# Performance work log

Measured on AMD Instinct MI355X. Metric: run time of the kernel, lower is better.

## Reference

```python
import jax, jax.numpy as jnp
import numpy as np

B, S, T = 64, 128, 64
HD, VS, VT = 1024, 32000, 32000


def setup_inputs() -> dict:
    key = jax.random.key(0)
    ks = jax.random.split(key, 20)
    p = lambda k, shape: (jax.random.normal(k, shape, jnp.float32) * 0.02)
    return {
        "src_nums": jax.random.randint(ks[0], (B, S), 0, VS, dtype=jnp.int32),
        "tgt_nums": jax.random.randint(ks[1], (B, T), 0, VT, dtype=jnp.int32),
        "src_emb": p(ks[2], (VS, HD)),
        "tgt_emb": p(ks[3], (VT, HD)),
        "enc_Wx1": p(ks[4], (HD, 4 * HD)),
        "enc_Wh1": p(ks[5], (HD, 4 * HD)),
        "enc_b1": jnp.zeros((4 * HD,), jnp.float32),
        "enc_Wx2": p(ks[6], (HD, 4 * HD)),
        "enc_Wh2": p(ks[7], (HD, 4 * HD)),
        "enc_b2": jnp.zeros((4 * HD,), jnp.float32),
        "dec_Wx": p(ks[8], (HD, 4 * HD)),
        "dec_Wh": p(ks[9], (HD, 4 * HD)),
        "dec_b": jnp.zeros((4 * HD,), jnp.float32),
        "dec_h0": p(ks[10], (1, HD)),
        "dec_m0": p(ks[11], (1, HD)),
        "Wt": p(ks[12], (2 * HD, HD)),
        "bt": jnp.zeros((HD,), jnp.float32),
        "Wo": p(ks[13], (HD, VT)),
        "bo": jnp.zeros((VT,), jnp.float32),
    }


def _lstm_cell(x, h, c, Wx, Wh, b):
    g = x @ Wx + h @ Wh + b            # [B, 4H], gate order i,f,g,o
    i, f, gg, o = jnp.split(g, 4, axis=-1)
    c = jax.nn.sigmoid(f) * c + jax.nn.sigmoid(i) * jnp.tanh(gg)
    h = jax.nn.sigmoid(o) * jnp.tanh(c)
    return h, c


def reference(src_nums, tgt_nums, src_emb, tgt_emb,
              enc_Wx1, enc_Wh1, enc_b1, enc_Wx2, enc_Wh2, enc_b2,
              dec_Wx, dec_Wh, dec_b, dec_h0, dec_m0, Wt, bt, Wo, bo):
    Bb, Ss = src_nums.shape
    Hd = src_emb.shape[1]
    # ---- Encoder: 2-layer LSTM over source ----
    embs = src_emb[src_nums]                       # [B,S,H]
    z0 = jnp.zeros((Bb, Hd), embs.dtype)

    def enc_step(carry, x):
        h1, c1, h2, c2 = carry
        h1, c1 = _lstm_cell(x, h1, c1, enc_Wx1, enc_Wh1, enc_b1)
        h2, c2 = _lstm_cell(h1, h2, c2, enc_Wx2, enc_Wh2, enc_b2)
        return (h1, c1, h2, c2), h2

    _, Hseq = jax.lax.scan(enc_step, (z0, z0, z0, z0), jnp.swapaxes(embs, 0, 1))
    Henc = jnp.swapaxes(Hseq, 0, 1)                # [B,S,H]
    mask = src_nums == 0                           # pad mask
    scale = 1.0 / jnp.sqrt(jnp.array(Hd, jnp.float32))

    # ---- Decoder: per-step attention + LSTMCell + tanh proj + log-softmax ----
    h = jnp.tile(dec_h0, (Bb, 1))
    m = jnp.tile(dec_m0, (Bb, 1))

    def dec_step(carry, tgt):
        h, m, loss = carry
        scores = jnp.einsum('bd,bsd->bs', h, Henc) * scale
        scores = jnp.where(mask, -jnp.inf, scores)
        a = jax.nn.softmax(scores, axis=-1)
        ctx = jnp.einsum('bs,bsd->bd', a, Henc)
        z = jnp.tanh(jnp.concatenate([ctx, h], axis=-1) @ Wt + bt)
        logp = jax.nn.log_softmax(z @ Wo + bo, axis=-1)    # [B,V]
        tok_lp = jnp.take_along_axis(logp, tgt[:, None], axis=-1)[:, 0]
        loss = loss - jnp.sum(jnp.where(tgt != 0, tok_lp, 0.0))
        x = tgt_emb[tgt]
        h, m = _lstm_cell(x, h, m, dec_Wx, dec_Wh, dec_b)
        return (h, m, loss), None

    (_, _, loss), _ = jax.lax.scan(
        dec_step, (h, m, jnp.float32(0.0)), jnp.swapaxes(tgt_nums, 0, 1))
    return loss
```

## Files before the change

kernel.cpp:

```cpp
#include <hip/hip_runtime.h>


#define Bv 64
#define Sv 128
#define Tv 64
#define Hv 1024
#define H4v 4096
#define Vv 32000
#define NBLK 256

using bf16x8 = __attribute__((ext_vector_type(8))) short;
using f32x4  = __attribute__((ext_vector_type(4))) float;

typedef __attribute__((address_space(1))) const void gvoid_t;
typedef __attribute__((address_space(3))) void lvoid_t;

__device__ __forceinline__ void gload16(const void* g, void* l) {
  __builtin_amdgcn_global_load_lds((gvoid_t*)g, (lvoid_t*)l, 16, 0, 0);
}

__device__ __forceinline__ float bf2f(unsigned short u) {
  unsigned int v = ((unsigned int)u) << 16;
  return __uint_as_float(v);
}
__device__ __forceinline__ unsigned short f2bf(float f) {
  unsigned int u = __float_as_uint(f);
  return (unsigned short)((u + 0x7FFFu + ((u >> 16) & 1u)) >> 16);
}
__device__ __forceinline__ float sigm(float x) { return 1.f / (1.f + __expf(-x)); }
__device__ __forceinline__ float tanh_f(float x) {
  float ax = fabsf(x);
  float e = __expf(-2.f * ax);
  float t = (1.f - e) / (1.f + e);
  return copysignf(t, x);
}

__device__ __forceinline__ int4 ldx4(const unsigned short* p) {
  int4 r;
  asm volatile("global_load_dwordx4 %0, %1, off" : "=v"(r) : "v"(p));
  return r;
}
__device__ __forceinline__ int2 ldx2(const unsigned short* p) {
  int2 r;
  asm volatile("global_load_dwordx2 %0, %1, off" : "=v"(r) : "v"(p));
  return r;
}
__device__ __forceinline__ void st_u16_wt(unsigned short* p, unsigned v) {
  asm volatile("global_store_short %0, %1, off sc0 sc1" :: "v"(p), "v"(v) : "memory");
}
__device__ __forceinline__ void vm_wait(int n) {
  if (n >= 12)     asm volatile("s_waitcnt vmcnt(12)" ::: "memory");
  else if (n >= 8) asm volatile("s_waitcnt vmcnt(8)" ::: "memory");
  else if (n >= 4) asm volatile("s_waitcnt vmcnt(4)" ::: "memory");
  else             asm volatile("s_waitcnt vmcnt(0)" ::: "memory");
}

__device__ __forceinline__ void wait_all64(int* f, int tid) {
  if (tid < 64) {
    int it = 0;
    while (true) {
      int v = __hip_atomic_load(f + tid, __ATOMIC_RELAXED, __HIP_MEMORY_SCOPE_AGENT);
      if (__all(v != 0)) break;
      __builtin_amdgcn_s_sleep(1);
      if (++it > (1 << 17)) break;
    }
  }
  __syncthreads();
}
__device__ __forceinline__ void wait_all128(int* f, int tid) {
  if (tid < 64) {
    int it = 0;
    while (true) {
      int a = __hip_atomic_load(f + tid, __ATOMIC_RELAXED, __HIP_MEMORY_SCOPE_AGENT);
      int b = __hip_atomic_load(f + tid + 64, __ATOMIC_RELAXED, __HIP_MEMORY_SCOPE_AGENT);
      if (__all((a != 0) && (b != 0))) break;
      __builtin_amdgcn_s_sleep(1);
      if (++it > (1 << 17)) break;
    }
  }
  __syncthreads();
}
__device__ __forceinline__ void post_flag(int* f, int tid) {
  __syncthreads();
  if (tid == 0) __hip_atomic_store(f, 1, __ATOMIC_RELAXED, __HIP_MEMORY_SCOPE_AGENT);
}

__global__ __launch_bounds__(256) void transpose_bf16(const float* __restrict__ in,
                                                      unsigned short* __restrict__ out,
                                                      int R, int C, int ostride) {
  __shared__ float tile[32][33];
  int tx = threadIdx.x, ty = threadIdx.y;
  int c0 = blockIdx.x * 32, r0 = blockIdx.y * 32;
#pragma unroll
  for (int i = 0; i < 32; i += 8)
    tile[ty + i][tx] = in[(size_t)(r0 + ty + i) * C + c0 + tx];
  __syncthreads();
#pragma unroll
  for (int i = 0; i < 32; i += 8)
    out[(size_t)(c0 + ty + i) * ostride + r0 + tx] = f2bf(tile[tx][ty + i]);
}

__global__ __launch_bounds__(256) void gather_emb(const int* __restrict__ toks,
                                                  const float* __restrict__ emb,
                                                  unsigned short* __restrict__ dst) {
  int r = blockIdx.x, tid = threadIdx.x;
  int tok = toks[r];
  int j = tid * 4;
  float4 v = *(const float4*)&emb[(size_t)tok * Hv + j];
  ushort4 o;
  o.x = f2bf(v.x); o.y = f2bf(v.y); o.z = f2bf(v.z); o.w = f2bf(v.w);
  *(ushort4*)&dst[(size_t)r * Hv + j] = o;
}

__global__ __launch_bounds__(256) void init_k(unsigned short* __restrict__ zhx,
                                              unsigned short* __restrict__ hdx0,
                                              const float* __restrict__ h0,
                                              int* __restrict__ flg) {
  int idx = blockIdx.x * 256 + threadIdx.x;
  int j = idx & (Hv - 1);
  int b = idx >> 10;
  zhx[idx] = 0;
  hdx0[(j >> 4) * 1024 + b * 16 + (j & 15)] = f2bf(h0[j]);
  if (idx < 28672) flg[idx] = 0;
}

template <int EPI>
__global__ __launch_bounds__(256) void gemm128(const unsigned short* __restrict__ A,
                                               const unsigned short* __restrict__ Bt,
                                               const float* __restrict__ bias,
                                               unsigned short* __restrict__ Cbf,
                                               int M, int N, int K,
                                               float* __restrict__ partial,
                                               float* __restrict__ tlog,
                                               const int* __restrict__ tgt) {
  __shared__ unsigned short As[128 * 64];
  __shared__ unsigned short Bs[128 * 64];
  int tid = threadIdx.x, lane = tid & 63, w = tid >> 6;
  int wr = w >> 1, wc = w & 1;
  int m0 = blockIdx.y * 128, n0 = blockIdx.x * 128;
  f32x4 acc[4][4] = {};
  for (int k0 = 0; k0 < K; k0 += 64) {
    __syncthreads();
#pragma unroll
    for (int q = 0; q < 4; ++q) {
      int idx = q * 256 + tid;
      int row = idx >> 3, phys = idx & 7, lg = phys ^ (row & 7);
      gload16(A + (size_t)(m0 + row) * K + k0 + lg * 8, &As[idx * 8]);
    }
#pragma unroll
    for (int q = 0; q < 4; ++q) {
      int idx = q * 256 + tid;
      int row = idx >> 3, phys = idx & 7, lg = phys ^ (row & 7);
      gload16(Bt + (size_t)(n0 + row) * K + k0 + lg * 8, &Bs[idx * 8]);
    }
    __syncthreads();
#pragma unroll
    for (int kk = 0; kk < 64; kk += 32) {
      int lgb = (kk >> 3) + (lane >> 4);
      bf16x8 af[4], bfr[4];
#pragma unroll
      for (int m = 0; m < 4; ++m) {
        int row = wr * 64 + m * 16 + (lane & 15);
        af[m] = *(const bf16x8*)&As[(row * 8 + (lgb ^ (row & 7))) * 8];
      }
#pragma unroll
      for (int n = 0; n < 4; ++n) {
        int row = wc * 64 + n * 16 + (lane & 15);
        bfr[n] = *(const bf16x8*)&Bs[(row * 8 + (lgb ^ (row & 7))) * 8];
      }
#pragma unroll
      for (int m = 0; m < 4; ++m)
#pragma unroll
        for (int n = 0; n < 4; ++n)
          acc[m][n] = __builtin_amdgcn_mfma_f32_16x16x32_bf16(af[m], bfr[n], acc[m][n], 0, 0, 0);
    }
  }
  if (EPI == 2) {
#pragma unroll
    for (int m = 0; m < 4; ++m)
#pragma unroll
      for (int n = 0; n < 4; ++n) {
        int col = n0 + wc * 64 + n * 16 + (lane & 15);
        float bv = bias[col];
#pragma unroll
        for (int j = 0; j < 4; ++j) {
          int row = m0 + wr * 64 + m * 16 + (lane >> 4) * 4 + j;
          float v = acc[m][n][j] + bv;
          Cbf[(size_t)row * N + col] = f2bf(tanhf(v));
        }
      }
  } else if (EPI == 3) {
    int chunk = (n0 + wc * 64) >> 6;
#pragma unroll
    for (int m = 0; m < 4; ++m)
#pragma unroll
      for (int j = 0; j < 4; ++j) {
        int row = m0 + wr * 64 + m * 16 + (lane >> 4) * 4 + j;
        int tv = tgt[row];
        float se = 0.f;
#pragma unroll
        for (int n = 0; n < 4; ++n) {
          int col = n0 + wc * 64 + n * 16 + (lane & 15);
          float v = acc[m][n][j] + bias[col];
          se += __expf(v);
          if (col == tv) tlog[row] = v;
        }
        se += __shfl_xor(se, 1);
        se += __shfl_xor(se, 2);
        se += __shfl_xor(se, 4);
        se += __shfl_xor(se, 8);
        if ((lane & 15) == 0) partial[(size_t)chunk * M + row] = se;
      }
  } else {
    constexpr int TTc = (EPI == 4) ? 128 : 64;
#pragma unroll
    for (int m = 0; m < 4; ++m)
#pragma unroll
      for (int n = 0; n < 4; ++n) {
        int col = n0 + wc * 64 + n * 16 + (lane & 15);
        float bv = bias[col];
        int hcol = col & 1023, g = col >> 10;
#pragma unroll
        for (int j = 0; j < 4; ++j) {
          int row = m0 + wr * 64 + m * 16 + (lane >> 4) * 4 + j;
          int t = row % TTc, b = row / TTc;
          float v = acc[m][n][j] + bv;
          Cbf[((((size_t)t * 64 + (hcol >> 4)) * 64 + b) * 16 + (hcol & 15)) * 4 + g] = f2bf(v);
        }
      }
  }
}

template <int GRP>
__device__ __forceinline__ void run6(
    int gid, int tid, const unsigned short* __restrict__ Wg,
    const unsigned short* __restrict__ XPC, const float* __restrict__ eb2,
    const float* __restrict__ m0, const unsigned short* __restrict__ ZHX,
    unsigned short* __restrict__ H1X, unsigned short* __restrict__ H2X,
    unsigned short* __restrict__ HDX,
    int* __restrict__ C1, int* __restrict__ C2, int* __restrict__ CD,
    unsigned short* Wl, float* gl) {
  constexpr int COLS = (GRP == 1) ? 8 : 16;
  constexpr int KD   = (GRP == 1) ? 2048 : 1024;
  constexpr int NKS  = KD / 128;
  constexpr int NFR  = (GRP == 1) ? 2 : 4;
  constexpr int NT   = (GRP == 2) ? 63 : 128;
  constexpr int GPR  = KD / 8;
  constexpr int WROWS = 4 * COLS;
  const int lane = tid & 63, w = tid >> 6, l4 = lane >> 4, l15 = lane & 15;
  const int j0 = gid * COLS;

#pragma unroll
  for (int it = 0; it < (WROWS * GPR) / 256; ++it) {
    int L = it * 256 + tid;
    int row = L / GPR;
    int g = (L % GPR) ^ (row & 7);
    int gate = row / COLS, cl = row % COLS;
    gload16(Wg + (size_t)(gate * 1024 + j0 + cl) * KD + g * 8, Wl + (size_t)L * 8);
  }
  const int rr0 = (GRP == 1) ? (tid >> 3) : (tid >> 4);
  const int cc  = (GRP == 1) ? (tid & 7) : (tid & 15);
  const bool cellact = (GRP != 1) || (tid < 128);
  float cst[4];
#pragma unroll
  for (int c = 0; c < 4; ++c) cst[c] = (GRP == 2) ? m0[j0 + cc] : 0.f;
  float br_[4];
  if (GRP == 1) {
#pragma unroll
    for (int g = 0; g < 4; ++g) br_[g] = eb2[g * 1024 + j0 + cc];
  }
  const int kq16 = w * (KD / 32);

  asm volatile("s_waitcnt vmcnt(0)" ::: "memory");
  __syncthreads();

  for (int t = 0; t < NT; ++t) {
    if (GRP == 0) {
      if (t > 0) wait_all64(C1 + (t - 1) * 64, tid);
    } else if (GRP == 1) {
      wait_all64(C1 + t * 64, tid);
      if (t > 0) wait_all128(C2 + (t - 1) * 128, tid);
    } else {
      if (t > 0) wait_all64(CD + t * 64, tid);
    }
    const unsigned short* slab;
    int jb;
    if (GRP == 0) {
      slab = (t == 0) ? ZHX : H1X + (size_t)(t - 1) * 65536;
      jb = w * 256;
    } else if (GRP == 2) {
      slab = HDX + (size_t)t * 65536;
      jb = w * 256;
    } else {
      if (w < 2) { slab = H1X + (size_t)t * 65536; jb = w * 512; }
      else {
        slab = (t == 0) ? ZHX : H2X + (size_t)(t - 1) * 65536;
        jb = w * 512 - 1024;
      }
    }
    int2 xq[4];
    if (GRP != 1) {
      const unsigned short* xb = XPC + ((size_t)t * 64 + gid) * 4096;
#pragma unroll
      for (int c = 0; c < 4; ++c) xq[c] = ldx2(xb + ((c * 16 + rr0) * 16 + cc) * 4);
    }
    const unsigned short* rp[4];
#pragma unroll
    for (int m = 0; m < 4; ++m)
      rp[m] = slab + (size_t)((jb >> 4) + (l4 >> 1)) * 1024 + (m * 16 + l15) * 16 + (l4 & 1) * 8;
    int4 afr[3][4];
#pragma unroll
    for (int pk = 0; pk < 3; ++pk)
#pragma unroll
      for (int m = 0; m < 4; ++m) afr[pk][m] = ldx4(rp[m] + pk * 2048);
    if (GRP != 1) vm_wait(12);
    bf16x8 wb[2][NFR];
#pragma unroll
    for (int n = 0; n < NFR; ++n) {
      int row = n * 16 + l15;
      wb[0][n] = *(const bf16x8*)&Wl[(size_t)row * KD + (size_t)((kq16 + l4) ^ (row & 7)) * 8];
    }
    f32x4 acc[4][NFR] = {};
#pragma unroll
    for (int ks = 0; ks < NKS; ++ks) {
      if (ks + 1 < NKS) {
#pragma unroll
        for (int n = 0; n < NFR; ++n) {
          int row = n * 16 + l15;
          wb[(ks + 1) & 1][n] = *(const bf16x8*)&Wl[(size_t)row * KD +
              (size_t)((kq16 + (ks + 1) * 4 + l4) ^ (row & 7)) * 8];
        }
      }
      int nrem = 4 * (NKS - 1 - ks);
      vm_wait(nrem > 8 ? 8 : nrem);
      __builtin_amdgcn_sched_barrier(0);
#pragma unroll
      for (int m = 0; m < 4; ++m)
#pragma unroll
        for (int n = 0; n < NFR; ++n)
          acc[m][n] = __builtin_amdgcn_mfma_f32_16x16x32_bf16(
              *(const bf16x8*)&afr[ks % 3][m], wb[ks & 1][n], acc[m][n], 0, 0, 0);
      if (ks + 3 < NKS) {
#pragma unroll
        for (int m = 0; m < 4; ++m) afr[ks % 3][m] = ldx4(rp[m] + (ks + 3) * 2048);
      }
    }
    unsigned short* outp;
    if (GRP == 0)      outp = H1X + (size_t)t * 65536 + gid * 1024;
    else if (GRP == 2) outp = HDX + (size_t)(t + 1) * 65536 + gid * 1024;
    else               outp = H2X + (size_t)t * 65536 + (size_t)(j0 >> 4) * 1024 + (j0 & 8);
#pragma unroll
    for (int c = 0; c < 4; ++c) {
#pragma unroll
      for (int n = 0; n < NFR; ++n)
#pragma unroll
        for (int j = 0; j < 4; ++j) {
          int ric = l4 * 4 + j;
          int col = n * 16 + l15;
          gl[(w * 16 + ric) * 64 + (col ^ ((ric * 4) & 63))] = acc[c][n][j];
        }
      __syncthreads();
      if (cellact) {
        float G[4];
#pragma unroll
        for (int g = 0; g < 4; ++g) {
          int sw = (g * COLS + cc) ^ ((rr0 * 4) & 63);
          G[g] = gl[(0 * 16 + rr0) * 64 + sw] + gl[(1 * 16 + rr0) * 64 + sw] +
                 gl[(2 * 16 + rr0) * 64 + sw] + gl[(3 * 16 + rr0) * 64 + sw];
        }
        float gi, gf, gg, go;
        if (GRP == 1) {
          gi = G[0] + br_[0]; gf = G[1] + br_[1]; gg = G[2] + br_[2]; go = G[3] + br_[3];
        } else {
          gi = G[0] + bf2f((unsigned short)(xq[c].x & 0xFFFF));
          gf = G[1] + bf2f((unsigned short)((unsigned)xq[c].x >> 16));
          gg = G[2] + bf2f((unsigned short)(xq[c].y & 0xFFFF));
          go = G[3] + bf2f((unsigned short)((unsigned)xq[c].y >> 16));
        }
        float cn = sigm(gf) * cst[c] + sigm(gi) * tanh_f(gg);
        float hn = sigm(go) * tanh_f(cn);
        cst[c] = cn;
        st_u16_wt(outp + (c * 16 + rr0) * 16 + cc, (unsigned)f2bf(hn));
      }
      __syncthreads();
    }
    asm volatile("s_waitcnt vmcnt(0)" ::: "memory");
    if (GRP == 0)      post_flag(C1 + t * 64 + gid, tid);
    else if (GRP == 1) post_flag(C2 + t * 128 + gid, tid);
    else               post_flag(CD + (t + 1) * 64 + gid, tid);
  }
}

__global__ __launch_bounds__(256, 1) void chain_kernel(
    const unsigned short* __restrict__ W1T, const unsigned short* __restrict__ W2S,
    const unsigned short* __restrict__ WDT, const unsigned short* __restrict__ XPC1,
    const unsigned short* __restrict__ XPCD, const float* __restrict__ eb2,
    const float* __restrict__ m0, const unsigned short* __restrict__ ZHX,
    unsigned short* __restrict__ H1X, unsigned short* __restrict__ H2X,
    unsigned short* __restrict__ HDX, int* __restrict__ flg) {
  __shared__ unsigned short Wl[65536];
  __shared__ float gl[4 * 16 * 64];
  int bid = blockIdx.x, tid = threadIdx.x;
  int* C1 = flg;
  int* C2 = flg + 8192;
  int* CD = flg + 24576;
  if (bid < 64)
    run6<0>(bid, tid, W1T, XPC1, eb2, nullptr, ZHX, H1X, H2X, HDX, C1, C2, CD, Wl, gl);
  else if (bid < 192)
    run6<1>(bid - 64, tid, W2S, nullptr, eb2, nullptr, ZHX, H1X, H2X, HDX, C1, C2, CD, Wl, gl);
  else
    run6<2>(bid - 192, tid, WDT, XPCD, eb2, m0, ZHX, H1X, H2X, HDX, C1, C2, CD, Wl, gl);
}

__global__ __launch_bounds__(256) void reshape_h(const unsigned short* __restrict__ H2X,
                                                 const unsigned short* __restrict__ HDX,
                                                 unsigned short* __restrict__ HENC,
                                                 unsigned short* __restrict__ HDEC) {
  int row = blockIdx.x, tid = threadIdx.x;
  int g = tid >> 2, c = (tid & 3) * 4;
  if (row < Bv * Sv) {
    int b = row >> 7, s = row & 127;
    ushort4 v = *(const ushort4*)&H2X[(size_t)s * 65536 + g * 1024 + b * 16 + c];
    *(ushort4*)&HENC[(size_t)row * Hv + tid * 4] = v;
  } else {
    int r2 = row - Bv * Sv;
    int b = r2 >> 6, t = r2 & 63;
    ushort4 v = *(const ushort4*)&HDX[(size_t)t * 65536 + g * 1024 + b * 16 + c];
    *(ushort4*)&HDEC[(size_t)r2 * Hv + tid * 4] = v;
  }
}

__global__ __launch_bounds__(256) void attn_kernel(const unsigned short* __restrict__ Hdec,
                                                   const unsigned short* __restrict__ Henc,
                                                   const int* __restrict__ src_nums,
                                                   unsigned short* __restrict__ cat) {
  __shared__ float hd[Hv];
  __shared__ float sc[Sv];
  __shared__ float al[Sv];
  __shared__ float inv_s;
  int r = blockIdx.x;
  int b = r >> 6;
  int tid = threadIdx.x;
#pragma unroll
  for (int i = 0; i < 4; ++i) {
    int j = i * 256 + tid;
    hd[j] = bf2f(Hdec[(size_t)r * Hv + j]);
  }
  __syncthreads();
  int lane = tid & 63, w = tid >> 6;
  {
    int s = w * 32 + (lane >> 1);
    int half = lane & 1;
    const unsigned short* hrow = Henc + ((size_t)(b * Sv + s)) * Hv + half * 512;
    const float* hdp = hd + half * 512;
    float ps = 0.f;
#pragma unroll 8
    for (int j = 0; j < 512; j += 2) {
      unsigned int u = *(const unsigned int*)&hrow[j];
      ps += hdp[j] * bf2f((unsigned short)(u & 0xFFFFu));
      ps += hdp[j + 1] * bf2f((unsigned short)(u >> 16));
    }
    ps += __shfl_xor(ps, 1);
    if (half == 0) {
      float v = ps * 0.03125f;
      if (src_nums[b * Sv + s] == 0) v = -1e30f;
      sc[s] = v;
    }
  }
  __syncthreads();
  if (w == 0) {
    float v0 = sc[lane], v1 = sc[lane + 64];
    float mx = fmaxf(v0, v1);
#pragma unroll
    for (int o = 1; o < 64; o <<= 1) mx = fmaxf(mx, __shfl_xor(mx, o));
    float e0 = __expf(v0 - mx), e1 = __expf(v1 - mx);
    al[lane] = e0;
    al[lane + 64] = e1;
    float ss = e0 + e1;
#pragma unroll
    for (int o = 1; o < 64; o <<= 1) ss += __shfl_xor(ss, o);
    if (lane == 0) inv_s = 1.f / ss;
  }
  __syncthreads();
  float inv = inv_s;
  int j0 = tid * 4;
  float a0 = 0, a1 = 0, a2 = 0, a3 = 0;
  for (int s2 = 0; s2 < Sv; ++s2) {
    float a = al[s2];
    const unsigned short* hr = Henc + ((size_t)(b * Sv + s2)) * Hv + j0;
    ushort4 u = *(const ushort4*)hr;
    a0 += a * bf2f(u.x);
    a1 += a * bf2f(u.y);
    a2 += a * bf2f(u.z);
    a3 += a * bf2f(u.w);
  }
  ushort4 o4;
  o4.x = f2bf(a0 * inv); o4.y = f2bf(a1 * inv); o4.z = f2bf(a2 * inv); o4.w = f2bf(a3 * inv);
  *(ushort4*)&cat[(size_t)r * 2048 + j0] = o4;
  ushort4 h4;
  h4.x = f2bf(hd[j0]); h4.y = f2bf(hd[j0 + 1]); h4.z = f2bf(hd[j0 + 2]); h4.w = f2bf(hd[j0 + 3]);
  *(ushort4*)&cat[(size_t)r * 2048 + 1024 + j0] = h4;
}

__global__ __launch_bounds__(256) void loss_row(const float* __restrict__ partial,
                                                const float* __restrict__ tlog,
                                                const int* __restrict__ tgt,
                                                float* __restrict__ rowloss) {
  int r = blockIdx.x * 256 + threadIdx.x;
  float ssum = 0.f;
  for (int c = 0; c < Vv / 64; ++c) ssum += partial[(size_t)c * (Bv * Tv) + r];
  float l = logf(ssum) - tlog[r];
  rowloss[r] = (tgt[r] != 0) ? l : 0.f;
}

__global__ __launch_bounds__(256) void loss_final(const float* __restrict__ rowloss,
                                                  float* __restrict__ out) {
  __shared__ float red[256];
  int tid = threadIdx.x;
  float s = 0.f;
  for (int i = tid; i < Bv * Tv; i += 256) s += rowloss[i];
  red[tid] = s;
  __syncthreads();
  for (int o = 128; o > 0; o >>= 1) {
    if (tid < o) red[tid] += red[tid + o];
    __syncthreads();
  }
  if (tid == 0) out[0] = red[0];
}

extern "C" void kernel_launch(void* const* d_in, const int* in_sizes, int n_in,
                              void* d_out, int out_size, void* d_ws, size_t ws_size,
                              hipStream_t stream) {
  (void)in_sizes; (void)n_in; (void)out_size; (void)ws_size;
  const int* src_nums = (const int*)d_in[0];
  const int* tgt_nums = (const int*)d_in[1];
  const float* src_emb = (const float*)d_in[2];
  const float* tgt_emb = (const float*)d_in[3];
  const float* eWx1 = (const float*)d_in[4];
  const float* eWh1 = (const float*)d_in[5];
  const float* eb1  = (const float*)d_in[6];
  const float* eWx2 = (const float*)d_in[7];
  const float* eWh2 = (const float*)d_in[8];
  const float* eb2  = (const float*)d_in[9];
  const float* dWx  = (const float*)d_in[10];
  const float* dWh  = (const float*)d_in[11];
  const float* db   = (const float*)d_in[12];
  const float* h0   = (const float*)d_in[13];
  const float* m0   = (const float*)d_in[14];
  const float* Wt   = (const float*)d_in[15];
  const float* bt   = (const float*)d_in[16];
  const float* Wo   = (const float*)d_in[17];
  const float* bo   = (const float*)d_in[18];

  char* base = (char*)d_ws;
  size_t off = 0;
  auto alloc = [&](size_t bytes) -> void* {
    void* r = base + off;
    off += (bytes + 255) & ~(size_t)255;
    return r;
  };
  unsigned short* WX1T = (unsigned short*)alloc((size_t)H4v * Hv * 2);
  unsigned short* W1T  = (unsigned short*)alloc((size_t)H4v * Hv * 2);
  unsigned short* W2S  = (unsigned short*)alloc((size_t)H4v * 2048 * 2);
  unsigned short* DWXT = (unsigned short*)alloc((size_t)H4v * Hv * 2);
  unsigned short* WDT  = (unsigned short*)alloc((size_t)H4v * Hv * 2);
  unsigned short* WTT  = (unsigned short*)alloc((size_t)Hv * 2048 * 2);
  unsigned short* WOT  = (unsigned short*)alloc((size_t)Vv * Hv * 2);
  unsigned short* SEMB = (unsigned short*)alloc((size_t)Bv * Sv * Hv * 2);
  unsigned short* TEMB = (unsigned short*)alloc((size_t)Bv * Tv * Hv * 2);
  unsigned short* XPC1 = (unsigned short*)alloc((size_t)Bv * Sv * H4v * 2);
  unsigned short* XPCD = (unsigned short*)alloc((size_t)Bv * Tv * H4v * 2);
  unsigned short* HENC = (unsigned short*)alloc((size_t)Bv * Sv * Hv * 2);
  unsigned short* HDEC = (unsigned short*)alloc((size_t)Bv * Tv * Hv * 2);
  unsigned short* H1X  = (unsigned short*)alloc((size_t)Sv * Bv * Hv * 2);
  unsigned short* H2X  = (unsigned short*)alloc((size_t)Sv * Bv * Hv * 2);
  unsigned short* HDX  = (unsigned short*)alloc((size_t)Tv * Bv * Hv * 2);
  unsigned short* ZHX  = (unsigned short*)alloc((size_t)Bv * Hv * 2);
  unsigned short* CAT  = (unsigned short*)alloc((size_t)Bv * Tv * 2048 * 2);
  unsigned short* ZBUF = (unsigned short*)alloc((size_t)Bv * Tv * Hv * 2);
  float* PART  = (float*)alloc((size_t)(Vv / 64) * (Bv * Tv) * 4);
  float* TLOG  = (float*)alloc((size_t)(Bv * Tv) * 4);
  float* RLOSS = (float*)alloc((size_t)(Bv * Tv) * 4);
  int* FLG     = (int*)alloc(28672 * 4);

  dim3 tb(32, 8);
  transpose_bf16<<<dim3(H4v / 32, Hv / 32), tb, 0, stream>>>(eWx1, WX1T, Hv, H4v, Hv);
  transpose_bf16<<<dim3(H4v / 32, Hv / 32), tb, 0, stream>>>(eWh1, W1T, Hv, H4v, Hv);
  transpose_bf16<<<dim3(H4v / 32, Hv / 32), tb, 0, stream>>>(eWx2, W2S, Hv, H4v, 2048);
  transpose_bf16<<<dim3(H4v / 32, Hv / 32), tb, 0, stream>>>(eWh2, W2S + 1024, Hv, H4v, 2048);
  transpose_bf16<<<dim3(H4v / 32, Hv / 32), tb, 0, stream>>>(dWx, DWXT, Hv, H4v, Hv);
  transpose_bf16<<<dim3(H4v / 32, Hv / 32), tb, 0, stream>>>(dWh, WDT, Hv, H4v, Hv);
  transpose_bf16<<<dim3(Hv / 32, 2048 / 32), tb, 0, stream>>>(Wt, WTT, 2048, Hv, 2048);
  transpose_bf16<<<dim3(Vv / 32, Hv / 32), tb, 0, stream>>>(Wo, WOT, Hv, Vv, Hv);

  init_k<<<256, 256, 0, stream>>>(ZHX, HDX, h0, FLG);
  gather_emb<<<Bv * Sv, 256, 0, stream>>>(src_nums, src_emb, SEMB);
  gather_emb<<<Bv * Tv, 256, 0, stream>>>(tgt_nums, tgt_emb, TEMB);

  gemm128<4><<<dim3(H4v / 128, (Bv * Sv) / 128), 256, 0, stream>>>(
      SEMB, WX1T, eb1, XPC1, Bv * Sv, H4v, Hv, nullptr, nullptr, nullptr);
  gemm128<5><<<dim3(H4v / 128, (Bv * Tv) / 128), 256, 0, stream>>>(
      TEMB, DWXT, db, XPCD, Bv * Tv, H4v, Hv, nullptr, nullptr, nullptr);

  chain_kernel<<<NBLK, 256, 0, stream>>>(W1T, W2S, WDT, XPC1, XPCD, eb2, m0, ZHX, H1X, H2X,
                                         HDX, FLG);

  reshape_h<<<Bv * Sv + Bv * Tv, 256, 0, stream>>>(H2X, HDX, HENC, HDEC);

  attn_kernel<<<Bv * Tv, 256, 0, stream>>>(HDEC, HENC, src_nums, CAT);
  gemm128<2><<<dim3(Hv / 128, (Bv * Tv) / 128), 256, 0, stream>>>(
      CAT, WTT, bt, ZBUF, Bv * Tv, Hv, 2048, nullptr, nullptr, nullptr);
  gemm128<3><<<dim3(Vv / 128, (Bv * Tv) / 128), 256, 0, stream>>>(
      ZBUF, WOT, bo, nullptr, Bv * Tv, Vv, Hv, PART, TLOG, tgt_nums);
  loss_row<<<(Bv * Tv) / 256, 256, 0, stream>>>(PART, TLOG, tgt_nums, RLOSS);
  loss_final<<<1, 256, 0, stream>>>(RLOSS, (float*)d_out);
}
```

Before: 1.832 ms.

## Deepen recurrent A-operand prefetch to eight stages and coalesce hidden-state stores

Inside the persistent LSTM chain kernel, the A-fragment prefetch ring for the recurrent matmul grows from three to eight k-slices, and the vmcnt waits are recomputed to match, so more global loads are in flight on the serial per-timestep critical path. The per-thread 16-bit write-through stores of new hidden values are replaced by staging them in LDS and issuing packed 8-byte write-through stores. This costs more registers for the deeper ring and adds an extra LDS round trip and barrier per step.

```diff
diff --git a/kernel.cpp b/kernel.cpp
--- a/kernel.cpp
+++ b/kernel.cpp
@@ -45,14 +45,20 @@
   asm volatile("global_load_dwordx2 %0, %1, off" : "=v"(r) : "v"(p));
   return r;
 }
-__device__ __forceinline__ void st_u16_wt(unsigned short* p, unsigned v) {
-  asm volatile("global_store_short %0, %1, off sc0 sc1" :: "v"(p), "v"(v) : "memory");
-}
-__device__ __forceinline__ void vm_wait(int n) {
-  if (n >= 12)     asm volatile("s_waitcnt vmcnt(12)" ::: "memory");
-  else if (n >= 8) asm volatile("s_waitcnt vmcnt(8)" ::: "memory");
-  else if (n >= 4) asm volatile("s_waitcnt vmcnt(4)" ::: "memory");
-  else             asm volatile("s_waitcnt vmcnt(0)" ::: "memory");
+__device__ __forceinline__ void stx2u_wt(unsigned short* p, int2 v) {
+  asm volatile("global_store_dwordx2 %0, %1, off sc0 sc1" :: "v"(p), "v"(v) : "memory");
+}
+__device__ __forceinline__ void vm_wait_c(int n) {
+  switch (n) {
+    case 28: asm volatile("s_waitcnt vmcnt(28)" ::: "memory"); break;
+    case 24: asm volatile("s_waitcnt vmcnt(24)" ::: "memory"); break;
+    case 20: asm volatile("s_waitcnt vmcnt(20)" ::: "memory"); break;
+    case 16: asm volatile("s_waitcnt vmcnt(16)" ::: "memory"); break;
+    case 12: asm volatile("s_waitcnt vmcnt(12)" ::: "memory"); break;
+    case 8:  asm volatile("s_waitcnt vmcnt(8)"  ::: "memory"); break;
+    case 4:  asm volatile("s_waitcnt vmcnt(4)"  ::: "memory"); break;
+    default: asm volatile("s_waitcnt vmcnt(0)"  ::: "memory"); break;
+  }
 }
 
 __device__ __forceinline__ void wait_all64(int* f, int tid) {
@@ -232,7 +238,7 @@
 }
 
 template <int GRP>
-__device__ __forceinline__ void run6(
+__device__ __forceinline__ void run7(
     int gid, int tid, const unsigned short* __restrict__ Wg,
     const unsigned short* __restrict__ XPC, const float* __restrict__ eb2,
     const float* __restrict__ m0, const unsigned short* __restrict__ ZHX,
@@ -308,12 +314,11 @@
 #pragma unroll
     for (int m = 0; m < 4; ++m)
       rp[m] = slab + (size_t)((jb >> 4) + (l4 >> 1)) * 1024 + (m * 16 + l15) * 16 + (l4 & 1) * 8;
-    int4 afr[3][4];
-#pragma unroll
-    for (int pk = 0; pk < 3; ++pk)
+    int4 afr[8][4];
+#pragma unroll
+    for (int pk = 0; pk < 8; ++pk)
 #pragma unroll
       for (int m = 0; m < 4; ++m) afr[pk][m] = ldx4(rp[m] + pk * 2048);
-    if (GRP != 1) vm_wait(12);
     bf16x8 wb[2][NFR];
 #pragma unroll
     for (int n = 0; n < NFR; ++n) {
@@ -331,24 +336,24 @@
               (size_t)((kq16 + (ks + 1) * 4 + l4) ^ (row & 7)) * 8];
         }
       }
-      int nrem = 4 * (NKS - 1 - ks);
-      vm_wait(nrem > 8 ? 8 : nrem);
+      vm_wait_c((GRP == 1) ? (ks <= 8 ? 28 : 60 - 4 * ks) : (28 - 4 * ks));
       __builtin_amdgcn_sched_barrier(0);
 #pragma unroll
       for (int m = 0; m < 4; ++m)
 #pragma unroll
         for (int n = 0; n < NFR; ++n)
           acc[m][n] = __builtin_amdgcn_mfma_f32_16x16x32_bf16(
-              *(const bf16x8*)&afr[ks % 3][m], wb[ks & 1][n], acc[m][n], 0, 0, 0);
-      if (ks + 3 < NKS) {
-#pragma unroll
-        for (int m = 0; m < 4; ++m) afr[ks % 3][m] = ldx4(rp[m] + (ks + 3) * 2048);
+              *(const bf16x8*)&afr[ks & 7][m], wb[ks & 1][n], acc[m][n], 0, 0, 0);
+      if (GRP == 1 && ks < 8) {
+#pragma unroll
+        for (int m = 0; m < 4; ++m) afr[ks & 7][m] = ldx4(rp[m] + (ks + 8) * 2048);
       }
     }
     unsigned short* outp;
     if (GRP == 0)      outp = H1X + (size_t)t * 65536 + gid * 1024;
     else if (GRP == 2) outp = HDX + (size_t)(t + 1) * 65536 + gid * 1024;
     else               outp = H2X + (size_t)t * 65536 + (size_t)(j0 >> 4) * 1024 + (j0 & 8);
+    unsigned short ho[4];
 #pragma unroll
     for (int c = 0; c < 4; ++c) {
 #pragma unroll
@@ -380,9 +385,30 @@
         float cn = sigm(gf) * cst[c] + sigm(gi) * tanh_f(gg);
         float hn = sigm(go) * tanh_f(cn);
         cst[c] = cn;
-        st_u16_wt(outp + (c * 16 + rr0) * 16 + cc, (unsigned)f2bf(hn));
+        ho[c] = f2bf(hn);
       }
       __syncthreads();
+    }
+    unsigned short* hb = (unsigned short*)gl;
+    if (cellact) {
+#pragma unroll
+      for (int c = 0; c < 4; ++c) hb[(c * 16 + rr0) * COLS + cc] = ho[c];
+    }
+    __syncthreads();
+    if (GRP != 1) {
+      int b2 = tid >> 2, q4 = (tid & 3) * 4;
+      ushort4 hv = *(const ushort4*)&hb[b2 * 16 + q4];
+      int2 pk;
+      pk.x = (int)hv.x | ((int)hv.y << 16);
+      pk.y = (int)hv.z | ((int)hv.w << 16);
+      stx2u_wt(outp + b2 * 16 + q4, pk);
+    } else if (tid < 128) {
+      int b2 = tid >> 1, q4 = (tid & 1) * 4;
+      ushort4 hv = *(const ushort4*)&hb[b2 * 8 + q4];
+      int2 pk;
+      pk.x = (int)hv.x | ((int)hv.y << 16);
+      pk.y = (int)hv.z | ((int)hv.w << 16);
+      stx2u_wt(outp + b2 * 16 + q4, pk);
     }
     asm volatile("s_waitcnt vmcnt(0)" ::: "memory");
     if (GRP == 0)      post_flag(C1 + t * 64 + gid, tid);
@@ -405,11 +431,11 @@
   int* C2 = flg + 8192;
   int* CD = flg + 24576;
   if (bid < 64)
-    run6<0>(bid, tid, W1T, XPC1, eb2, nullptr, ZHX, H1X, H2X, HDX, C1, C2, CD, Wl, gl);
+    run7<0>(bid, tid, W1T, XPC1, eb2, nullptr, ZHX, H1X, H2X, HDX, C1, C2, CD, Wl, gl);
   else if (bid < 192)
-    run6<1>(bid - 64, tid, W2S, nullptr, eb2, nullptr, ZHX, H1X, H2X, HDX, C1, C2, CD, Wl, gl);
+    run7<1>(bid - 64, tid, W2S, nullptr, eb2, nullptr, ZHX, H1X, H2X, HDX, C1, C2, CD, Wl, gl);
   else
-    run6<2>(bid - 192, tid, WDT, XPCD, eb2, m0, ZHX, H1X, H2X, HDX, C1, C2, CD, Wl, gl);
+    run7<2>(bid - 192, tid, WDT, XPCD, eb2, m0, ZHX, H1X, H2X, HDX, C1, C2, CD, Wl, gl);
 }
 
 __global__ __launch_bounds__(256) void reshape_h(const unsigned short* __restrict__ H2X,
```

Measured after the change: 1.831 ms. Within noise of the previous version (-0.1%).
